# Optimization experiments

Hardware: AMD Instinct MI355X
Metric: run time of the kernel (lower is better)

Reference implementation:

```python
import jax, jax.numpy as jnp
import numpy as np

B, S, H = 4, 2048, 1024
E, K = 8, 2

def setup_inputs() -> dict:
    key = jax.random.key(0)
    ks = jax.random.split(key, 5)
    scale = 1.0 / np.sqrt(H)
    return {
        "x": jax.random.normal(ks[0], (B, S, H), dtype=jnp.float32),
        "router_w": jax.random.uniform(ks[1], (E, H), jnp.float32, -scale, scale),
        "router_b": jax.random.uniform(ks[2], (E,), jnp.float32, -scale, scale),
        "expert_w": jax.random.uniform(ks[3], (E, H, H), jnp.float32, -scale, scale),
        "expert_b": jax.random.uniform(ks[4], (E, H), jnp.float32, -scale, scale),
    }


def reference(x, router_w, router_b, expert_w, expert_b):
    # Router: [b,s,E]
    scores = jnp.einsum("bsh,eh->bse", x, router_w) + router_b
    probs = jax.nn.softmax(scores, axis=-1)
    p, expert_id = jax.lax.top_k(probs, K)          # [b,s,K]
    # Renormalize top-k probs (matches p / p.sum(dim=2))
    p = p / jnp.sum(p, axis=-1, keepdims=True)
    # Per-token combine weight per expert: [b,s,E]
    onehot = jax.nn.one_hot(expert_id, E, dtype=x.dtype)  # [b,s,K,E]
    w_comb = jnp.einsum("bske,bsk->bse", onehot, p)
    # All-expert linear (Linear: x @ W.T + b): [b,s,E,h]
    all_out = jnp.einsum("bsh,edh->bsed", x, expert_w) + expert_b
    # Weighted combine over selected experts: [b,s,h]
    return jnp.einsum("bse,bsed->bsd", w_comb, all_out)
```

## Files before the change

kernel.cpp:

```cpp
#include <hip/hip_runtime.h>
#include <hip/hip_bf16.h>
#include <math.h>

#define TOK 8192
#define HD 1024
#define NE 8
#define SLOTS 18432
#define NGRP 512
#define GRPSZ 16

typedef _Float16 half8 __attribute__((ext_vector_type(8)));
typedef _Float16 half4v __attribute__((ext_vector_type(4)));
typedef float floatx4 __attribute__((ext_vector_type(4)));

#define WAIT_VMCNT0() asm volatile("s_waitcnt vmcnt(0)" ::: "memory")
#define WAIT_LGKM0()  asm volatile("s_waitcnt lgkmcnt(0)" ::: "memory")

__global__ __launch_bounds__(256) void score_cvt(
    const float* __restrict__ x,
    const float* __restrict__ rw,
    const float* __restrict__ rb,
    const float* __restrict__ ew,
    _Float16* __restrict__ xh,
    _Float16* __restrict__ wh,
    int* __restrict__ epair,
    float* __restrict__ w1out,
    int* __restrict__ hist) {
  const int tid = threadIdx.x;
  const int blk = blockIdx.x;
  if (blk >= NGRP) {
    const int g = (blk - NGRP) * 256 + tid;
    const float4* src = (const float4*)ew;
    half4v* dst = (half4v*)wh;
#pragma unroll
    for (int j = 0; j < 4; ++j) {
      float4 v = src[g + 524288 * j];
      half4v h = {(_Float16)v.x, (_Float16)v.y, (_Float16)v.z, (_Float16)v.w};
      dst[g + 524288 * j] = h;
    }
    return;
  }
  const int lane = tid & 63;
  const int wid = tid >> 6;
  __shared__ int hcnt[NE];
  if (tid < NE) hcnt[tid] = 0;
  __syncthreads();

#pragma unroll
  for (int i = 0; i < 4; ++i) {
    const int t = blk * GRPSZ + wid * 4 + i;
    const float4* xp = (const float4*)(x + (size_t)t * HD);
    float4 xr[4];
#pragma unroll
    for (int k = 0; k < 4; ++k) xr[k] = xp[lane + 64 * k];
    _Float16* xo = xh + (size_t)t * HD;
#pragma unroll
    for (int k = 0; k < 4; ++k) {
      half4v h = {(_Float16)xr[k].x, (_Float16)xr[k].y,
                  (_Float16)xr[k].z, (_Float16)xr[k].w};
      *(half4v*)(xo + (lane + 64 * k) * 4) = h;
    }
    float sc[NE];
#pragma unroll
    for (int e = 0; e < NE; ++e) {
      const float4* wp = (const float4*)(rw + e * HD);
      float a = 0.f;
#pragma unroll
      for (int k = 0; k < 4; ++k) {
        float4 w = wp[lane + 64 * k];
        a += xr[k].x * w.x + xr[k].y * w.y + xr[k].z * w.z + xr[k].w * w.w;
      }
#pragma unroll
      for (int off = 32; off > 0; off >>= 1) a += __shfl_xor(a, off);
      sc[e] = a + rb[e];
    }
    float b1 = sc[0]; int e1 = 0;
#pragma unroll
    for (int e = 1; e < NE; ++e) if (sc[e] > b1) { b1 = sc[e]; e1 = e; }
    float b2 = -1e30f; int e2 = 0;
#pragma unroll
    for (int e = 0; e < NE; ++e) { if (e != e1 && sc[e] > b2) { b2 = sc[e]; e2 = e; } }
    if (lane == 0) {
      epair[t] = e1 | (e2 << 8);
      w1out[t] = 1.f / (1.f + expf(b2 - b1));
      atomicAdd(&hcnt[e1], 1);
      atomicAdd(&hcnt[e2], 1);
    }
  }
  __syncthreads();
  if (tid < NE) hist[tid * NGRP + blk] = hcnt[tid];
}

__global__ __launch_bounds__(256) void moe_scatter(
    const int* __restrict__ hist,
    const int* __restrict__ epair,
    const float* __restrict__ w1in,
    int* __restrict__ cntp,
    int* __restrict__ basep,
    int* __restrict__ tok_list,
    float* __restrict__ tok_w,
    int* __restrict__ slot_of) {
  const int tid = threadIdx.x;
  const int blk = blockIdx.x;
  __shared__ int pre_s[NE], tot_s[NE], alloc_s[NE];
  {
    const int e = tid >> 5;
    const int sl = tid & 31;
    int p = 0, tt = 0;
#pragma unroll
    for (int j = 0; j < 16; ++j) {
      int g = sl + 32 * j;
      int h = hist[e * NGRP + g];
      tt += h;
      p += (g < blk) ? h : 0;
    }
#pragma unroll
    for (int off = 16; off > 0; off >>= 1) {
      p += __shfl_xor(p, off);
      tt += __shfl_xor(tt, off);
    }
    if (sl == 0) { pre_s[e] = p; tot_s[e] = tt; }
  }
  __syncthreads();
  if (tid == 0) {
    int b = 0;
    for (int e = 0; e < NE; ++e) {
      alloc_s[e] = b + pre_s[e];
      if (blk == 0) { cntp[e * 64] = tot_s[e]; basep[e] = b; }
      b += (tot_s[e] + 255) & ~255;
    }
  }
  __syncthreads();
  if (tid < GRPSZ) {
    const int t = blk * GRPSZ + tid;
    int ep = epair[t];
    int e1 = ep & 0xff, e2 = ep >> 8;
    float w1 = w1in[t];
    int s1 = atomicAdd(&alloc_s[e1], 1);
    tok_list[s1] = t; tok_w[s1] = w1; slot_of[2 * t] = s1;
    int s2 = atomicAdd(&alloc_s[e2], 1);
    tok_list[s2] = t; tok_w[s2] = 1.f - w1; slot_of[2 * t + 1] = s2;
  }
}

template <int EPI>
__global__ __launch_bounds__(512, 2) void moe_gemm(
    const _Float16* __restrict__ Ah, const _Float16* __restrict__ Bh,
    const float* __restrict__ eb,
    const int* __restrict__ cntp, const int* __restrict__ base,
    const int* __restrict__ tok_list, const float* __restrict__ tok_w,
    _Float16* __restrict__ scratch, float* __restrict__ out) {
  const int e = blockIdx.x;
  const int ce = cntp[e * 64];
  const int m0 = (blockIdx.y >> 2) << 8;
  if (m0 >= ce) return;
  const int nb = (blockIdx.y & 3) << 8;
  const int sbase = base[e];
  const int tid = threadIdx.x;
  const int lane = tid & 63;
  const int wid = tid >> 6;
  const int wm = wid >> 2, wn = wid & 3;

  __shared__ _Float16 A_s[2][256 * 64];
  __shared__ _Float16 B_s[2][256 * 64];
  __shared__ int tok_s[256];
  __shared__ float w_s[256];

  if (tid < 256) {
    int tk = 0; float w = 0.f;
    if (m0 + tid < ce) { tk = tok_list[sbase + m0 + tid]; w = tok_w[sbase + m0 + tid]; }
    tok_s[tid] = tk; w_s[tid] = w;
  }
  __syncthreads();

  floatx4 acc[8][4];
  floatx4 zero = {0.f, 0.f, 0.f, 0.f};
#pragma unroll
  for (int i = 0; i < 8; ++i)
#pragma unroll
    for (int j = 0; j < 4; ++j) acc[i][j] = zero;

  const int wbase = e * HD * HD;
  const int rloc = lane >> 3, sub = lane & 7;
  const int g8 = (sub ^ rloc) * 8;
  int agoff[4], bgoff[4];
#pragma unroll
  for (int u = 0; u < 4; ++u) {
    const int row = u * 64 + wid * 8 + rloc;
    agoff[u] = tok_s[row] * HD + g8;
    bgoff[u] = wbase + (nb + row) * HD + g8;
  }
  const int l15 = lane & 15, q4 = lane >> 4;
  const int ck0 = ((q4)     ^ (l15 & 7)) * 8;
  const int ck1 = ((4 + q4) ^ (l15 & 7)) * 8;
  const int arow0 = (wm * 128 + l15) * 64;
  const int brow0 = (wn * 64  + l15) * 64;

  auto stageA = [&](int buf, int k0) {
#pragma unroll
    for (int u = 0; u < 4; ++u) {
      const int r0 = u * 64 + wid * 8;
      __builtin_amdgcn_global_load_lds(
          (const __attribute__((address_space(1))) unsigned int*)(Ah + agoff[u] + k0),
          (__attribute__((address_space(3))) unsigned int*)&A_s[buf][r0 * 64], 16, 0, 0);
    }
  };
  auto stageB = [&](int buf, int k0) {
#pragma unroll
    for (int u = 0; u < 4; ++u) {
      const int r0 = u * 64 + wid * 8;
      __builtin_amdgcn_global_load_lds(
          (const __attribute__((address_space(1))) unsigned int*)(Bh + bgoff[u] + k0),
          (__attribute__((address_space(3))) unsigned int*)&B_s[buf][r0 * 64], 16, 0, 0);
    }
  };

  stageA(0, 0);
  stageB(0, 0);
  WAIT_VMCNT0();
  __builtin_amdgcn_s_barrier();

#pragma unroll 2
  for (int t = 0; t < 16; ++t) {
    const int cur = t & 1, nxt = cur ^ 1;
    const int kn = (t + 1) * 64;
    half8 afr[4][2], b01[2][2], b23[2][2];

#pragma unroll
    for (int i = 0; i < 4; ++i) {
      afr[i][0] = *(const half8*)&A_s[cur][arow0 + i * 16 * 64 + ck0];
      afr[i][1] = *(const half8*)&A_s[cur][arow0 + i * 16 * 64 + ck1];
    }
#pragma unroll
    for (int j = 0; j < 2; ++j) {
      b01[j][0] = *(const half8*)&B_s[cur][brow0 + j * 16 * 64 + ck0];
      b01[j][1] = *(const half8*)&B_s[cur][brow0 + j * 16 * 64 + ck1];
    }
    if (t < 15) stageA(nxt, kn);
    __builtin_amdgcn_s_barrier();
    WAIT_LGKM0();
    __builtin_amdgcn_sched_barrier(0);
    __builtin_amdgcn_s_setprio(1);
#pragma unroll
    for (int i = 0; i < 4; ++i)
#pragma unroll
      for (int j = 0; j < 2; ++j) {
        acc[i][j] = __builtin_amdgcn_mfma_f32_16x16x32_f16(afr[i][0], b01[j][0], acc[i][j], 0, 0, 0);
        acc[i][j] = __builtin_amdgcn_mfma_f32_16x16x32_f16(afr[i][1], b01[j][1], acc[i][j], 0, 0, 0);
      }
    __builtin_amdgcn_s_setprio(0);
    __builtin_amdgcn_s_barrier();

#pragma unroll
    for (int j = 0; j < 2; ++j) {
      b23[j][0] = *(const half8*)&B_s[cur][brow0 + (j + 2) * 16 * 64 + ck0];
      b23[j][1] = *(const half8*)&B_s[cur][brow0 + (j + 2) * 16 * 64 + ck1];
    }
    if (t < 15) stageB(nxt, kn);
    __builtin_amdgcn_s_barrier();
    WAIT_LGKM0();
    __builtin_amdgcn_sched_barrier(0);
    __builtin_amdgcn_s_setprio(1);
#pragma unroll
    for (int i = 0; i < 4; ++i)
#pragma unroll
      for (int j = 0; j < 2; ++j) {
        acc[i][j + 2] = __builtin_amdgcn_mfma_f32_16x16x32_f16(afr[i][0], b23[j][0], acc[i][j + 2], 0, 0, 0);
        acc[i][j + 2] = __builtin_amdgcn_mfma_f32_16x16x32_f16(afr[i][1], b23[j][1], acc[i][j + 2], 0, 0, 0);
      }
    __builtin_amdgcn_s_setprio(0);
    __builtin_amdgcn_s_barrier();

#pragma unroll
    for (int i = 0; i < 4; ++i) {
      afr[i][0] = *(const half8*)&A_s[cur][arow0 + (i + 4) * 16 * 64 + ck0];
      afr[i][1] = *(const half8*)&A_s[cur][arow0 + (i + 4) * 16 * 64 + ck1];
    }
    __builtin_amdgcn_s_barrier();
    WAIT_LGKM0();
    __builtin_amdgcn_sched_barrier(0);
    __builtin_amdgcn_s_setprio(1);
#pragma unroll
    for (int i = 0; i < 4; ++i)
#pragma unroll
      for (int j = 0; j < 2; ++j) {
        acc[i + 4][j + 2] = __builtin_amdgcn_mfma_f32_16x16x32_f16(afr[i][0], b23[j][0], acc[i + 4][j + 2], 0, 0, 0);
        acc[i + 4][j + 2] = __builtin_amdgcn_mfma_f32_16x16x32_f16(afr[i][1], b23[j][1], acc[i + 4][j + 2], 0, 0, 0);
      }
    __builtin_amdgcn_s_setprio(0);
    __builtin_amdgcn_s_barrier();

    __builtin_amdgcn_s_setprio(1);
#pragma unroll
    for (int i = 0; i < 4; ++i)
#pragma unroll
      for (int j = 0; j < 2; ++j) {
        acc[i + 4][j] = __builtin_amdgcn_mfma_f32_16x16x32_f16(afr[i][0], b01[j][0], acc[i + 4][j], 0, 0, 0);
        acc[i + 4][j] = __builtin_amdgcn_mfma_f32_16x16x32_f16(afr[i][1], b01[j][1], acc[i + 4][j], 0, 0, 0);
      }
    __builtin_amdgcn_s_setprio(0);
    WAIT_VMCNT0();
    __builtin_amdgcn_s_barrier();
  }

#pragma unroll
  for (int j = 0; j < 4; ++j) {
    const int col = nb + wn * 64 + j * 16 + l15;
    const float bias = eb[e * HD + col];
#pragma unroll
    for (int i = 0; i < 8; ++i) {
      const int rbase = wm * 128 + i * 16 + (q4 << 2);
#pragma unroll
      for (int r = 0; r < 4; ++r) {
        const int row = rbase + r;
        const float v = w_s[row] * (acc[i][j][r] + bias);
        if (EPI == 1) {
          scratch[(size_t)(sbase + m0 + row) * HD + col] = (_Float16)v;
        } else {
          if (m0 + row < ce)
            atomicAdd(&out[(size_t)tok_s[row] * HD + col], v);
        }
      }
    }
  }
}

__global__ void moe_combine(const _Float16* __restrict__ scratch,
                            const int* __restrict__ slot_of,
                            float* __restrict__ out) {
  const int tid = threadIdx.x;
  const int t = blockIdx.x * 2 + (tid >> 7);
  const int c = (tid & 127) * 8;
  int sa = slot_of[2 * t], sb = slot_of[2 * t + 1];
  half8 a = *(const half8*)&scratch[(size_t)sa * HD + c];
  half8 b = *(const half8*)&scratch[(size_t)sb * HD + c];
  float* o = out + (size_t)t * HD + c;
  float4 o0 = {(float)a[0] + (float)b[0], (float)a[1] + (float)b[1],
               (float)a[2] + (float)b[2], (float)a[3] + (float)b[3]};
  float4 o1 = {(float)a[4] + (float)b[4], (float)a[5] + (float)b[5],
               (float)a[6] + (float)b[6], (float)a[7] + (float)b[7]};
  *(float4*)o = o0;
  *(float4*)(o + 4) = o1;
}

extern "C" void kernel_launch(void* const* d_in, const int* in_sizes, int n_in,
                              void* d_out, int out_size, void* d_ws, size_t ws_size,
                              hipStream_t stream) {
  (void)in_sizes; (void)n_in;
  const float* x  = (const float*)d_in[0];
  const float* rw = (const float*)d_in[1];
  const float* rb = (const float*)d_in[2];
  const float* ew = (const float*)d_in[3];
  const float* eb = (const float*)d_in[4];
  float* out = (float*)d_out;

  char* w = (char*)d_ws;
  int*   cntp     = (int*)(w + 0);
  int*   basep    = (int*)(w + 2048);
  int*   hist     = (int*)(w + 2304);
  size_t off = 2304 + (size_t)NE * NGRP * 4;
  int*   tok_list = (int*)(w + off);  off += (size_t)SLOTS * 4;
  float* tok_w    = (float*)(w + off); off += (size_t)SLOTS * 4;
  int*   slot_of  = (int*)(w + off);  off += (size_t)TOK * 8;
  int*   epair    = (int*)(w + off);  off += (size_t)TOK * 4;
  float* w1buf    = (float*)(w + off); off += (size_t)TOK * 4;
  off = (off + 255) & ~255ull;
  size_t xh_off = off;
  size_t wh_off = xh_off + (size_t)TOK * HD * 2;
  size_t scr_off = wh_off + (size_t)NE * HD * HD * 2;
  size_t needscr = scr_off + (size_t)SLOTS * HD * 2;
  bool fastscr = ws_size >= needscr;

  if (!fastscr)
    hipMemsetAsync(d_out, 0, (size_t)out_size * sizeof(float), stream);

  _Float16* xh = (_Float16*)(w + xh_off);
  _Float16* wh = (_Float16*)(w + wh_off);
  _Float16* scr = fastscr ? (_Float16*)(w + scr_off) : nullptr;

  score_cvt<<<NGRP + 2048, 256, 0, stream>>>(x, rw, rb, ew, xh, wh,
                                             epair, w1buf, hist);
  moe_scatter<<<NGRP, 256, 0, stream>>>(hist, epair, w1buf, cntp, basep,
                                        tok_list, tok_w, slot_of);

  dim3 grid(NE, 256, 1);
  if (fastscr) {
    moe_gemm<1><<<grid, 512, 0, stream>>>(xh, wh, eb, cntp, basep,
                                          tok_list, tok_w, scr, out);
    moe_combine<<<TOK / 2, 256, 0, stream>>>(scr, slot_of, out);
  } else {
    moe_gemm<0><<<grid, 512, 0, stream>>>(xh, wh, eb, cntp, basep,
                                          tok_list, tok_w, nullptr, out);
  }
}
```

Before: 210.4 us.

## Split GEMM tile loads into quarter-stages with finer vmcnt pipelining and remapped grid

New measurement: 202.2 us. -3.9%, faster.

```diff
diff --git a/kernel.cpp b/kernel.cpp
--- a/kernel.cpp
+++ b/kernel.cpp
@@ -13,8 +13,12 @@
 typedef _Float16 half4v __attribute__((ext_vector_type(4)));
 typedef float floatx4 __attribute__((ext_vector_type(4)));
 
-#define WAIT_VMCNT0() asm volatile("s_waitcnt vmcnt(0)" ::: "memory")
+#define WAIT_VMCNT(N) asm volatile("s_waitcnt vmcnt(" #N ")" ::: "memory")
 #define WAIT_LGKM0()  asm volatile("s_waitcnt lgkmcnt(0)" ::: "memory")
+#define MEMFENCE()    asm volatile("" ::: "memory")
+
+struct CTrue  { static constexpr bool value = true;  };
+struct CFalse { static constexpr bool value = false; };
 
 __global__ __launch_bounds__(256) void score_cvt(
     const float* __restrict__ x,
@@ -150,11 +154,13 @@
     const int* __restrict__ cntp, const int* __restrict__ base,
     const int* __restrict__ tok_list, const float* __restrict__ tok_w,
     _Float16* __restrict__ scratch, float* __restrict__ out) {
-  const int e = blockIdx.x;
+  const int ybl = blockIdx.y;
+  const int e = ybl >> 5;
+  const int mt = ybl & 31;
   const int ce = cntp[e * 64];
-  const int m0 = (blockIdx.y >> 2) << 8;
+  const int m0 = mt << 8;
   if (m0 >= ce) return;
-  const int nb = (blockIdx.y & 3) << 8;
+  const int nb = blockIdx.x << 8;
   const int sbase = base[e];
   const int tid = threadIdx.x;
   const int lane = tid & 63;
@@ -186,58 +192,64 @@
   int agoff[4], bgoff[4];
 #pragma unroll
   for (int u = 0; u < 4; ++u) {
-    const int row = u * 64 + wid * 8 + rloc;
+    const int row = (u >> 1) * 128 + wid * 16 + (u & 1) * 8 + rloc;
     agoff[u] = tok_s[row] * HD + g8;
     bgoff[u] = wbase + (nb + row) * HD + g8;
   }
   const int l15 = lane & 15, q4 = lane >> 4;
-  const int ck0 = ((q4)     ^ (l15 & 7)) * 8;
+  const int ck0 = (q4 ^ (l15 & 7)) * 8;
   const int ck1 = ((4 + q4) ^ (l15 & 7)) * 8;
-  const int arow0 = (wm * 128 + l15) * 64;
-  const int brow0 = (wn * 64  + l15) * 64;
-
-  auto stageA = [&](int buf, int k0) {
-#pragma unroll
-    for (int u = 0; u < 4; ++u) {
-      const int r0 = u * 64 + wid * 8;
-      __builtin_amdgcn_global_load_lds(
-          (const __attribute__((address_space(1))) unsigned int*)(Ah + agoff[u] + k0),
-          (__attribute__((address_space(3))) unsigned int*)&A_s[buf][r0 * 64], 16, 0, 0);
-    }
+
+  auto gl = [](const _Float16* src, _Float16* dst) {
+    __builtin_amdgcn_global_load_lds(
+        (const __attribute__((address_space(1))) unsigned int*)src,
+        (__attribute__((address_space(3))) unsigned int*)dst, 16, 0, 0);
   };
-  auto stageB = [&](int buf, int k0) {
-#pragma unroll
-    for (int u = 0; u < 4; ++u) {
-      const int r0 = u * 64 + wid * 8;
-      __builtin_amdgcn_global_load_lds(
-          (const __attribute__((address_space(1))) unsigned int*)(Bh + bgoff[u] + k0),
-          (__attribute__((address_space(3))) unsigned int*)&B_s[buf][r0 * 64], 16, 0, 0);
+  auto stageA = [&](int uh, int buf, int k0) {
+#pragma unroll
+    for (int c = 0; c < 2; ++c) {
+      const int r0 = uh * 128 + wid * 16 + c * 8;
+      gl(Ah + agoff[uh * 2 + c] + k0, &A_s[buf][r0 * 64]);
     }
   };
-
-  stageA(0, 0);
-  stageB(0, 0);
-  WAIT_VMCNT0();
-  __builtin_amdgcn_s_barrier();
-
-#pragma unroll 2
-  for (int t = 0; t < 16; ++t) {
+  auto stageB = [&](int uh, int buf, int k0) {
+#pragma unroll
+    for (int c = 0; c < 2; ++c) {
+      const int r0 = uh * 128 + wid * 16 + c * 8;
+      gl(Bh + bgoff[uh * 2 + c] + k0, &B_s[buf][r0 * 64]);
+    }
+  };
+  auto mf = [](half8 a, half8 b, floatx4 c) {
+    return __builtin_amdgcn_mfma_f32_16x16x32_f16(a, b, c, 0, 0, 0);
+  };
+
+  stageA(0, 0, 0);
+  stageB(0, 0, 0);
+  stageB(1, 0, 0);
+  stageA(1, 0, 0);
+
+  auto run_tile = [&](int t, auto lastc) {
+    constexpr bool LAST = decltype(lastc)::value;
     const int cur = t & 1, nxt = cur ^ 1;
     const int kn = (t + 1) * 64;
-    half8 afr[4][2], b01[2][2], b23[2][2];
-
+    half8 a0[4][2], a1[4][2], b01[2][2], b23[2][2];
+
+    if constexpr (!LAST) { stageA(0, nxt, kn); WAIT_VMCNT(6); }
+    else { WAIT_VMCNT(4); }
+    __builtin_amdgcn_s_barrier();
+    MEMFENCE();
 #pragma unroll
     for (int i = 0; i < 4; ++i) {
-      afr[i][0] = *(const half8*)&A_s[cur][arow0 + i * 16 * 64 + ck0];
-      afr[i][1] = *(const half8*)&A_s[cur][arow0 + i * 16 * 64 + ck1];
+      const int r = (wm * 64 + i * 16 + l15) * 64;
+      a0[i][0] = *(const half8*)&A_s[cur][r + ck0];
+      a0[i][1] = *(const half8*)&A_s[cur][r + ck1];
     }
 #pragma unroll
     for (int j = 0; j < 2; ++j) {
-      b01[j][0] = *(const half8*)&B_s[cur][brow0 + j * 16 * 64 + ck0];
-      b01[j][1] = *(const half8*)&B_s[cur][brow0 + j * 16 * 64 + ck1];
-    }
-    if (t < 15) stageA(nxt, kn);
-    __builtin_amdgcn_s_barrier();
+      const int r = (wn * 32 + j * 16 + l15) * 64;
+      b01[j][0] = *(const half8*)&B_s[cur][r + ck0];
+      b01[j][1] = *(const half8*)&B_s[cur][r + ck1];
+    }
     WAIT_LGKM0();
     __builtin_amdgcn_sched_barrier(0);
     __builtin_amdgcn_s_setprio(1);
@@ -245,19 +257,21 @@
     for (int i = 0; i < 4; ++i)
 #pragma unroll
       for (int j = 0; j < 2; ++j) {
-        acc[i][j] = __builtin_amdgcn_mfma_f32_16x16x32_f16(afr[i][0], b01[j][0], acc[i][j], 0, 0, 0);
-        acc[i][j] = __builtin_amdgcn_mfma_f32_16x16x32_f16(afr[i][1], b01[j][1], acc[i][j], 0, 0, 0);
+        acc[i][j] = mf(a0[i][0], b01[j][0], acc[i][j]);
+        acc[i][j] = mf(a0[i][1], b01[j][1], acc[i][j]);
       }
     __builtin_amdgcn_s_setprio(0);
+
+    if constexpr (!LAST) { stageB(0, nxt, kn); WAIT_VMCNT(6); }
+    else { WAIT_VMCNT(2); }
     __builtin_amdgcn_s_barrier();
-
+    MEMFENCE();
 #pragma unroll
     for (int j = 0; j < 2; ++j) {
-      b23[j][0] = *(const half8*)&B_s[cur][brow0 + (j + 2) * 16 * 64 + ck0];
-      b23[j][1] = *(const half8*)&B_s[cur][brow0 + (j + 2) * 16 * 64 + ck1];
-    }
-    if (t < 15) stageB(nxt, kn);
-    __builtin_amdgcn_s_barrier();
+      const int r = (128 + wn * 32 + j * 16 + l15) * 64;
+      b23[j][0] = *(const half8*)&B_s[cur][r + ck0];
+      b23[j][1] = *(const half8*)&B_s[cur][r + ck1];
+    }
     WAIT_LGKM0();
     __builtin_amdgcn_sched_barrier(0);
     __builtin_amdgcn_s_setprio(1);
@@ -265,18 +279,21 @@
     for (int i = 0; i < 4; ++i)
 #pragma unroll
       for (int j = 0; j < 2; ++j) {
-        acc[i][j + 2] = __builtin_amdgcn_mfma_f32_16x16x32_f16(afr[i][0], b23[j][0], acc[i][j + 2], 0, 0, 0);
-        acc[i][j + 2] = __builtin_amdgcn_mfma_f32_16x16x32_f16(afr[i][1], b23[j][1], acc[i][j + 2], 0, 0, 0);
+        acc[i][j + 2] = mf(a0[i][0], b23[j][0], acc[i][j + 2]);
+        acc[i][j + 2] = mf(a0[i][1], b23[j][1], acc[i][j + 2]);
       }
     __builtin_amdgcn_s_setprio(0);
+
+    if constexpr (!LAST) { stageB(1, nxt, kn); WAIT_VMCNT(6); }
+    else { WAIT_VMCNT(0); }
     __builtin_amdgcn_s_barrier();
-
+    MEMFENCE();
 #pragma unroll
     for (int i = 0; i < 4; ++i) {
-      afr[i][0] = *(const half8*)&A_s[cur][arow0 + (i + 4) * 16 * 64 + ck0];
-      afr[i][1] = *(const half8*)&A_s[cur][arow0 + (i + 4) * 16 * 64 + ck1];
-    }
-    __builtin_amdgcn_s_barrier();
+      const int r = (128 + wm * 64 + i * 16 + l15) * 64;
+      a1[i][0] = *(const half8*)&A_s[cur][r + ck0];
+      a1[i][1] = *(const half8*)&A_s[cur][r + ck1];
+    }
     WAIT_LGKM0();
     __builtin_amdgcn_sched_barrier(0);
     __builtin_amdgcn_s_setprio(1);
@@ -284,32 +301,33 @@
     for (int i = 0; i < 4; ++i)
 #pragma unroll
       for (int j = 0; j < 2; ++j) {
-        acc[i + 4][j + 2] = __builtin_amdgcn_mfma_f32_16x16x32_f16(afr[i][0], b23[j][0], acc[i + 4][j + 2], 0, 0, 0);
-        acc[i + 4][j + 2] = __builtin_amdgcn_mfma_f32_16x16x32_f16(afr[i][1], b23[j][1], acc[i + 4][j + 2], 0, 0, 0);
+        acc[i + 4][j + 2] = mf(a1[i][0], b23[j][0], acc[i + 4][j + 2]);
+        acc[i + 4][j + 2] = mf(a1[i][1], b23[j][1], acc[i + 4][j + 2]);
       }
     __builtin_amdgcn_s_setprio(0);
-    __builtin_amdgcn_s_barrier();
-
+
+    if constexpr (!LAST) stageA(1, nxt, kn);
     __builtin_amdgcn_s_setprio(1);
 #pragma unroll
     for (int i = 0; i < 4; ++i)
 #pragma unroll
       for (int j = 0; j < 2; ++j) {
-        acc[i + 4][j] = __builtin_amdgcn_mfma_f32_16x16x32_f16(afr[i][0], b01[j][0], acc[i + 4][j], 0, 0, 0);
-        acc[i + 4][j] = __builtin_amdgcn_mfma_f32_16x16x32_f16(afr[i][1], b01[j][1], acc[i + 4][j], 0, 0, 0);
+        acc[i + 4][j] = mf(a1[i][0], b01[j][0], acc[i + 4][j]);
+        acc[i + 4][j] = mf(a1[i][1], b01[j][1], acc[i + 4][j]);
       }
     __builtin_amdgcn_s_setprio(0);
-    WAIT_VMCNT0();
-    __builtin_amdgcn_s_barrier();
-  }
+  };
+
+  for (int t = 0; t < 15; ++t) run_tile(t, CFalse{});
+  run_tile(15, CTrue{});
 
 #pragma unroll
   for (int j = 0; j < 4; ++j) {
-    const int col = nb + wn * 64 + j * 16 + l15;
+    const int col = nb + wn * 32 + (j & 1) * 16 + (j >> 1) * 128 + l15;
     const float bias = eb[e * HD + col];
 #pragma unroll
     for (int i = 0; i < 8; ++i) {
-      const int rbase = wm * 128 + i * 16 + (q4 << 2);
+      const int rbase = wm * 64 + (i & 3) * 16 + (i >> 2) * 128 + (q4 << 2);
 #pragma unroll
       for (int r = 0; r < 4; ++r) {
         const int row = rbase + r;
@@ -383,7 +401,7 @@
   moe_scatter<<<NGRP, 256, 0, stream>>>(hist, epair, w1buf, cntp, basep,
                                         tok_list, tok_w, slot_of);
 
-  dim3 grid(NE, 256, 1);
+  dim3 grid(HD / 256, NE * 32, 1);
   if (fastscr) {
     moe_gemm<1><<<grid, 512, 0, stream>>>(xh, wh, eb, cntp, basep,
                                           tok_list, tok_w, scr, out);
```
